# Kernel tuning notes

Measured on AMD Instinct MI355X. Metric: run time of the kernel, lower is better.

## Reference

```python
import jax, jax.numpy as jnp
import numpy as np

ALPHA = 1.0  # DPMConfig.alpha
N, D, K = 4096, 256, 64


def setup_inputs() -> dict:
    key = jax.random.key(0)
    k1, k2, k3, k4 = jax.random.split(key, 4)
    x = jax.random.normal(k1, (N, D), dtype=jnp.float32)
    means = jax.random.normal(k2, (K, D), dtype=jnp.float32)
    # SPD covariances: A A^T / D + 0.5 I
    A = jax.random.normal(k3, (K, D, D), dtype=jnp.float32)
    covs = jnp.einsum('kde,kfe->kdf', A, A) / D + 0.5 * jnp.eye(D, dtype=jnp.float32)
    counts = jax.random.uniform(k4, (K,), dtype=jnp.float32, minval=1.0, maxval=200.0)
    n_points = 100000
    return {"x": x, "means": means, "covs": covs, "counts": counts, "n_points": n_points}


def reference(x, means, covs, counts, n_points):
    n, d = x.shape
    k = means.shape[0]
    # deviations from every cluster mean: [N, K, D]
    dev = x[:, None, :] - means[None, :, :]
    # batched Mahalanobis solve: covs broadcast over points
    solved = jnp.linalg.solve(covs[None], dev[..., None])[..., 0]  # [N, K, D]
    quad = jnp.sum(dev * solved, axis=-1)  # [N, K]
    # logdet with the same jitter as the original
    _, log_dets = jnp.linalg.slogdet(covs + 1e-10 * jnp.eye(d, dtype=covs.dtype))  # [K]
    log_lik = -0.5 * (d * jnp.log(2.0 * jnp.pi) + log_dets[None, :] + quad)  # [N, K]
    denom = jnp.asarray(n_points, jnp.float32) + ALPHA
    log_prior = jnp.log(counts / denom)  # [K]
    log_new = jnp.log(ALPHA / denom)
    log_probs = jnp.concatenate(
        [log_lik + log_prior[None, :], jnp.full((n, 1), log_new, dtype=x.dtype)], axis=1
    )  # [N, K+1]
    # stable normalize (max-subtract + exp + sum == softmax)
    probs = jax.nn.softmax(log_probs, axis=1)
    return probs
```

## Files before the change

### kernel.cpp

```cpp
#include <hip/hip_runtime.h>
#include <math.h>


#define DD 256
#define KC 64
#define NPTS 4096
#define NT 64
#define BB 64
#define KG 4
#define CH 8
#define NCH (DD / CH)

__global__ __launch_bounds__(512) void pivot_kernel(
    const float* __restrict__ covs, float* __restrict__ S,
    float* __restrict__ Plbuf, float* __restrict__ ldp, int bs)
{
  const int k = blockIdx.x;
  const int by = blockIdx.y;
  const int tid = threadIdx.x;
  float* Pb = Plbuf + (size_t)k * BB * BB;

  __shared__ __align__(16) float Tl[BB][BB + 4];
  __shared__ __align__(16) float pivc[2][BB];
  __shared__ __align__(16) float pivr[2][BB];

  if (by < 4) {
    if (bs == 0) return;
    const int j0p = (bs - 1) * BB;
    const int r0 = by * BB;
    const float* src = ((bs == 1) ? covs : (const float*)S) + (size_t)k * DD * DD;
    float* dst = S + (size_t)k * DD * DD;

    const int rr = tid >> 3;
    const int cc = (tid & 7) * 8;
    *reinterpret_cast<float4*>(&Tl[rr][cc]) =
        *reinterpret_cast<const float4*>(&Pb[rr * BB + cc]);
    *reinterpret_cast<float4*>(&Tl[rr][cc + 4]) =
        *reinterpret_cast<const float4*>(&Pb[rr * BB + cc + 4]);
    __syncthreads();

    const int r = r0 + rr;
    if (r0 == j0p) {
      *reinterpret_cast<float4*>(&dst[(size_t)r * DD + j0p + cc]) =
          *reinterpret_cast<const float4*>(&Tl[rr][cc]);
      *reinterpret_cast<float4*>(&dst[(size_t)r * DD + j0p + cc + 4]) =
          *reinterpret_cast<const float4*>(&Tl[rr][cc + 4]);
    } else {
      float Crow[BB];
      #pragma unroll
      for (int p = 0; p < BB; p += 4) {
        float4 cv = *reinterpret_cast<const float4*>(&src[(size_t)r * DD + j0p + p]);
        Crow[p] = cv.x; Crow[p + 1] = cv.y; Crow[p + 2] = cv.z; Crow[p + 3] = cv.w;
      }
      float acc[8] = {0.f, 0.f, 0.f, 0.f, 0.f, 0.f, 0.f, 0.f};
      #pragma unroll
      for (int p = 0; p < BB; ++p) {
        float4 t0 = *reinterpret_cast<const float4*>(&Tl[p][cc]);
        float4 t1 = *reinterpret_cast<const float4*>(&Tl[p][cc + 4]);
        acc[0] = fmaf(Crow[p], t0.x, acc[0]);
        acc[1] = fmaf(Crow[p], t0.y, acc[1]);
        acc[2] = fmaf(Crow[p], t0.z, acc[2]);
        acc[3] = fmaf(Crow[p], t0.w, acc[3]);
        acc[4] = fmaf(Crow[p], t1.x, acc[4]);
        acc[5] = fmaf(Crow[p], t1.y, acc[5]);
        acc[6] = fmaf(Crow[p], t1.z, acc[6]);
        acc[7] = fmaf(Crow[p], t1.w, acc[7]);
      }
      float4 o0 = {-acc[0], -acc[1], -acc[2], -acc[3]};
      float4 o1 = {-acc[4], -acc[5], -acc[6], -acc[7]};
      *reinterpret_cast<float4*>(&dst[(size_t)r * DD + j0p + cc]) = o0;
      *reinterpret_cast<float4*>(&dst[(size_t)r * DD + j0p + cc + 4]) = o1;
    }
    return;
  }

  if (bs == 4) return;

  const int j0 = bs * BB;
  const float* psrc = ((bs == 0) ? covs : (const float*)S) + (size_t)k * DD * DD;
  const int pr = tid >> 3;
  const int pc = (tid & 7) * 8;

  float v[8];
  {
    float4 a4 = *reinterpret_cast<const float4*>(&psrc[(size_t)(j0 + pr) * DD + j0 + pc]);
    float4 b4 = *reinterpret_cast<const float4*>(&psrc[(size_t)(j0 + pr) * DD + j0 + pc + 4]);
    v[0] = a4.x; v[1] = a4.y; v[2] = a4.z; v[3] = a4.w;
    v[4] = b4.x; v[5] = b4.y; v[6] = b4.z; v[7] = b4.w;
  }
  if (pc == 0) pivc[0][pr] = v[0];
  if (pr == 0) {
    #pragma unroll
    for (int e = 0; e < 8; ++e) pivr[0][pc + e] = v[e];
  }
  __syncthreads();

  float ld = 0.0f;
  #pragma unroll 1
  for (int p = 0; p < BB; ++p) {
    const int cur = p & 1, nxt = cur ^ 1;
    const float d = pivc[cur][p];
    const float inv_d = 1.0f / d;
    if (tid == 0) ld += logf(d);
    const float cr = pivc[cur][pr];
    float rw[8];
    *reinterpret_cast<float4*>(&rw[0]) = *reinterpret_cast<const float4*>(&pivr[cur][pc]);
    *reinterpret_cast<float4*>(&rw[4]) = *reinterpret_cast<const float4*>(&pivr[cur][pc + 4]);
    #pragma unroll
    for (int e = 0; e < 8; ++e) {
      float ge = fmaf(-inv_d * cr, rw[e], v[e]);
      if (pr == p)     ge = rw[e] * inv_d;
      if (pc + e == p) ge = (pr == p) ? -inv_d : cr * inv_d;
      v[e] = ge;
    }
    if (p < BB - 1) {
      if (pr == p + 1) {
        #pragma unroll
        for (int e = 0; e < 8; ++e) pivr[nxt][pc + e] = v[e];
      }
      if (pc <= p + 1 && p + 1 < pc + 8) pivc[nxt][pr] = v[p + 1 - pc];
    }
    __syncthreads();
  }

  float4 s0 = {v[0], v[1], v[2], v[3]};
  float4 s1 = {v[4], v[5], v[6], v[7]};
  *reinterpret_cast<float4*>(&Pb[pr * BB + pc]) = s0;
  *reinterpret_cast<float4*>(&Pb[pr * BB + pc + 4]) = s1;
  if (tid == 0) ldp[bs * KC + k] = ld;
}

__global__ __launch_bounds__(512) void update_kernel(
    const float* __restrict__ covs, float* __restrict__ S,
    const float* __restrict__ Plbuf, int bs)
{
  const int k = blockIdx.x;
  const int si = blockIdx.y;
  const int t = si + (si >= bs ? 1 : 0);
  const int c0 = t * BB;
  const int j0 = bs * BB;
  const int tid = threadIdx.x;
  const float* src = ((bs == 0) ? covs : (const float*)S) + (size_t)k * DD * DD;
  float* dst = S + (size_t)k * DD * DD;

  __shared__ __align__(16) float Pl[BB][BB + 4];
  __shared__ __align__(16) float SJ[BB][BB + 4];
  __shared__ __align__(16) float Tl[BB][BB + 4];

  const float* Pb = Plbuf + (size_t)k * BB * BB;
  #pragma unroll
  for (int q = 0; q < 8; ++q) {
    int e = q * 512 + tid;
    int r = e >> 6, c = e & 63;
    Pl[r][c] = Pb[e];
    SJ[r][c] = src[(size_t)(j0 + r) * DD + c0 + c];
  }
  __syncthreads();

  {
    const int c = tid & 63;
    const int rg = (tid >> 6) * 8;
    float tv[8];
    #pragma unroll
    for (int r = 0; r < 8; ++r) tv[r] = 0.0f;
    for (int p = 0; p < BB; p += 4) {
      float s0 = SJ[p][c], s1 = SJ[p + 1][c], s2 = SJ[p + 2][c], s3 = SJ[p + 3][c];
      #pragma unroll
      for (int r = 0; r < 8; ++r) {
        float4 pv = *reinterpret_cast<const float4*>(&Pl[rg + r][p]);
        tv[r] = fmaf(pv.x, s0, fmaf(pv.y, s1, fmaf(pv.z, s2, fmaf(pv.w, s3, tv[r]))));
      }
    }
    #pragma unroll
    for (int r = 0; r < 8; ++r) Tl[rg + r][c] = tv[r];
  }
  __syncthreads();

  const int r = tid & 255;
  const int h = (tid >> 8) * 32;
  const bool inJ = (r >= j0) && (r < j0 + BB);
  if (inJ) {
    #pragma unroll
    for (int c = 0; c < 32; c += 4) {
      float4 tv4 = *reinterpret_cast<const float4*>(&Tl[r - j0][h + c]);
      float4 o = {-tv4.x, -tv4.y, -tv4.z, -tv4.w};
      *reinterpret_cast<float4*>(&dst[(size_t)r * DD + c0 + h + c]) = o;
    }
  } else {
    float Crow[BB];
    #pragma unroll
    for (int p = 0; p < BB; p += 4) {
      float4 cv = *reinterpret_cast<const float4*>(&src[(size_t)r * DD + j0 + p]);
      Crow[p] = cv.x; Crow[p + 1] = cv.y; Crow[p + 2] = cv.z; Crow[p + 3] = cv.w;
    }
    #pragma unroll
    for (int c = 0; c < 32; c += 4) {
      float4 acc = *reinterpret_cast<const float4*>(&src[(size_t)r * DD + c0 + h + c]);
      #pragma unroll
      for (int p = 0; p < BB; ++p) {
        float4 tv4 = *reinterpret_cast<const float4*>(&Tl[p][h + c]);
        acc.x = fmaf(Crow[p], tv4.x, acc.x);
        acc.y = fmaf(Crow[p], tv4.y, acc.y);
        acc.z = fmaf(Crow[p], tv4.z, acc.z);
        acc.w = fmaf(Crow[p], tv4.w, acc.w);
      }
      *reinterpret_cast<float4*>(&dst[(size_t)r * DD + c0 + h + c]) = acc;
    }
  }
}

__global__ __launch_bounds__(256) void w_kernel(
    const float* __restrict__ S, const float* __restrict__ means,
    const float* __restrict__ counts, const int* __restrict__ n_points_p,
    const float* __restrict__ ldp, float* __restrict__ cA,
    float* __restrict__ wv)
{
  const int k = blockIdx.x;
  const int tid = threadIdx.x;
  if (tid == 0) {
    float denom = (float)(*n_points_p) + 1.0f;
    float ld = ldp[k] + ldp[KC + k] + ldp[2 * KC + k] + ldp[3 * KC + k];
    cA[k] = logf(counts[k] / denom) - 0.5f * (470.49652900079047f + ld);
  }
  const float* Sk = S + (size_t)k * DD * DD;
  __shared__ float mus[DD];
  mus[tid] = means[(size_t)k * DD + tid];
  __syncthreads();
  float a0 = 0.f, a1 = 0.f, a2 = 0.f, a3 = 0.f;
  for (int j = 0; j < DD; j += 4) {
    a0 = fmaf(Sk[(size_t)(j + 0) * DD + tid], mus[j + 0], a0);
    a1 = fmaf(Sk[(size_t)(j + 1) * DD + tid], mus[j + 1], a1);
    a2 = fmaf(Sk[(size_t)(j + 2) * DD + tid], mus[j + 2], a2);
    a3 = fmaf(Sk[(size_t)(j + 3) * DD + tid], mus[j + 3], a3);
  }
  wv[(size_t)k * DD + tid] = (a0 + a1) + (a2 + a3);
}

__global__ __launch_bounds__(256) void quad_kernel(
    const float* __restrict__ X, const float* __restrict__ means,
    const float* __restrict__ S, const float* __restrict__ cA,
    const float* __restrict__ wv, float* __restrict__ lp)
{
  __shared__ __align__(16) float XT[DD][NT];
  __shared__ __align__(16) float Pl[CH * DD];
  __shared__ __align__(16) float muw[2][DD];
  __shared__ __align__(16) float lpb[KG][NT];

  const int tid = threadIdx.x;
  const int n0 = blockIdx.x * NT;
  const int k0 = blockIdx.y * KG;

  #pragma unroll
  for (int q = 0; q < 16; ++q) {
    int f = q * 1024 + tid * 4;
    int r = f >> 8;
    int c = f & 255;
    float4 xv = *reinterpret_cast<const float4*>(X + (size_t)(n0 + r) * DD + c);
    int rs = r ^ (((c >> 2) & 15) << 2);
    XT[c + 0][rs] = xv.x;
    XT[c + 1][rs] = xv.y;
    XT[c + 2][rs] = xv.z;
    XT[c + 3][rs] = xv.w;
  }

  const int tn = tid & 7;
  const int tj = tid >> 3;
  const int f0 = tid * 4;
  const int f1 = 1024 + tid * 4;

  #pragma unroll 1
  for (int kk = 0; kk < KG; ++kk) {
    const int k = k0 + kk;
    const float* Sk = S + (size_t)k * DD * DD;

    __syncthreads();
    muw[0][tid] = means[(size_t)k * DD + tid];
    muw[1][tid] = wv[(size_t)k * DD + tid];

    float4 pre0 = *reinterpret_cast<const float4*>(Sk + f0);
    float4 pre1 = *reinterpret_cast<const float4*>(Sk + f1);

    float y[8][8];
    #pragma unroll
    for (int a = 0; a < 8; ++a)
      #pragma unroll
      for (int b = 0; b < 8; ++b) y[a][b] = 0.0f;

    #pragma unroll 1
    for (int ct = 0; ct < NCH; ++ct) {
      __syncthreads();
      *reinterpret_cast<float4*>(&Pl[f0]) = pre0;
      *reinterpret_cast<float4*>(&Pl[f1]) = pre1;
      if (ct < NCH - 1) {
        const float* srcp = Sk + (size_t)(ct + 1) * CH * DD;
        pre0 = *reinterpret_cast<const float4*>(srcp + f0);
        pre1 = *reinterpret_cast<const float4*>(srcp + f1);
      }
      __syncthreads();

      #pragma unroll
      for (int il = 0; il < CH; ++il) {
        const int i = ct * CH + il;
        const int sw = ((i >> 2) & 15) << 2;
        float xv[8], pv[8];
        *reinterpret_cast<float4*>(&xv[0]) =
            *reinterpret_cast<const float4*>(&XT[i][(tn * 8) ^ sw]);
        *reinterpret_cast<float4*>(&xv[4]) =
            *reinterpret_cast<const float4*>(&XT[i][(tn * 8 + 4) ^ sw]);
        *reinterpret_cast<float4*>(&pv[0]) =
            *reinterpret_cast<const float4*>(&Pl[il * DD + tj * 8]);
        *reinterpret_cast<float4*>(&pv[4]) =
            *reinterpret_cast<const float4*>(&Pl[il * DD + tj * 8 + 4]);
        #pragma unroll
        for (int a = 0; a < 8; ++a)
          #pragma unroll
          for (int b = 0; b < 8; ++b)
            y[a][b] = fmaf(xv[a], pv[b], y[a][b]);
      }
    }

    float s[8];
    #pragma unroll
    for (int a = 0; a < 8; ++a) s[a] = 0.0f;
    #pragma unroll
    for (int b = 0; b < 8; ++b) {
      const int j = tj * 8 + b;
      const int swj = ((j >> 2) & 15) << 2;
      float dv[8];
      *reinterpret_cast<float4*>(&dv[0]) =
          *reinterpret_cast<const float4*>(&XT[j][(tn * 8) ^ swj]);
      *reinterpret_cast<float4*>(&dv[4]) =
          *reinterpret_cast<const float4*>(&XT[j][(tn * 8 + 4) ^ swj]);
      const float mj = muw[0][j];
      const float wj = muw[1][j];
      #pragma unroll
      for (int a = 0; a < 8; ++a)
        s[a] = fmaf(dv[a] - mj, y[a][b] - wj, s[a]);
    }

    float* qred = &Pl[0];
    __syncthreads();
    *reinterpret_cast<float4*>(&qred[tj * 64 + tn * 8]) =
        *reinterpret_cast<const float4*>(&s[0]);
    *reinterpret_cast<float4*>(&qred[tj * 64 + tn * 8 + 4]) =
        *reinterpret_cast<const float4*>(&s[4]);
    __syncthreads();
    if (tid < 64) {
      float qa = 0.f, qb = 0.f, qc = 0.f, qd = 0.f;
      #pragma unroll
      for (int t = 0; t < 32; t += 4) {
        qa += qred[(t + 0) * 64 + tid];
        qb += qred[(t + 1) * 64 + tid];
        qc += qred[(t + 2) * 64 + tid];
        qd += qred[(t + 3) * 64 + tid];
      }
      lpb[kk][tid] = fmaf(0.5f, (qa + qb) + (qc + qd), cA[k]);
    }
  }

  __syncthreads();
  if (tid < 64) {
    float4 o = {lpb[0][tid], lpb[1][tid], lpb[2][tid], lpb[3][tid]};
    *reinterpret_cast<float4*>(&lp[(size_t)(n0 + tid) * KC + k0]) = o;
  }
}

__global__ __launch_bounds__(64) void softmax_kernel(
    const float* __restrict__ lp, const int* __restrict__ n_points_p,
    float* __restrict__ out)
{
  const int n = blockIdx.x;
  const int l = threadIdx.x;
  const float denom = (float)(*n_points_p) + 1.0f;
  const float log_new = -logf(denom);

  float v = lp[(size_t)n * KC + l];
  float m = v;
  #pragma unroll
  for (int off = 32; off > 0; off >>= 1) m = fmaxf(m, __shfl_xor(m, off, 64));
  m = fmaxf(m, log_new);

  float e = expf(v - m);
  float s = e;
  #pragma unroll
  for (int off = 32; off > 0; off >>= 1) s += __shfl_xor(s, off, 64);
  float enew = expf(log_new - m);
  s += enew;

  out[(size_t)n * (KC + 1) + l] = e / s;
  if (l == 0) out[(size_t)n * (KC + 1) + KC] = enew / s;
}

extern "C" void kernel_launch(void* const* d_in, const int* in_sizes, int n_in,
                              void* d_out, int out_size, void* d_ws, size_t ws_size,
                              hipStream_t stream)
{
  const float* x       = (const float*)d_in[0];
  const float* means   = (const float*)d_in[1];
  const float* covs    = (const float*)d_in[2];
  const float* counts  = (const float*)d_in[3];
  const int*   n_points = (const int*)d_in[4];

  float* S   = (float*)d_ws;
  float* cA  = S + (size_t)KC * DD * DD;
  float* ldp = cA + KC;
  float* lp  = ldp + 4 * KC;
  float* Plbuf = lp;
  float* out = (float*)d_out;
  float* wv = out;

  for (int bs = 0; bs < 4; ++bs) {
    pivot_kernel<<<dim3(KC, 5), 512, 0, stream>>>(covs, S, Plbuf, ldp, bs);
    update_kernel<<<dim3(KC, 3), 512, 0, stream>>>(covs, S, Plbuf, bs);
  }
  pivot_kernel<<<dim3(KC, 5), 512, 0, stream>>>(covs, S, Plbuf, ldp, 4);
  w_kernel<<<KC, 256, 0, stream>>>(S, means, counts, n_points, ldp, cA, wv);
  quad_kernel<<<dim3(NPTS / NT, KC / KG), 256, 0, stream>>>(x, means, S, cA, wv, lp);
  softmax_kernel<<<NPTS, 64, 0, stream>>>(lp, n_points, out);
}
```

Measured before the change: 648.2 us.

## Fuse blocked covariance inversion sweep and w computation into one cooperative kernel

Replaces the nine pivot/update kernel launches and the separate w_kernel with a single cooperative kernel of 4 blocks per cluster, using grid-wide syncs between phases. Each block redundantly computes the 64x64 pivot inverse in shared memory, so the pivot block no longer round-trips through a global buffer and the per-step log-determinants accumulate in registers. The w = S*mu product is also split across the 4 blocks per cluster instead of one. This removes launch gaps and global staging at the cost of duplicated pivot work, grid-sync latency, and a co-residency requirement of 256 blocks of 512 threads.

```diff
diff --git a/kernel.cpp b/kernel.cpp
--- a/kernel.cpp
+++ b/kernel.cpp
@@ -1,5 +1,8 @@
 #include <hip/hip_runtime.h>
+#include <hip/hip_cooperative_groups.h>
 #include <math.h>
+
+namespace cg = cooperative_groups;
 
 
 #define DD 256
@@ -11,229 +14,217 @@
 #define CH 8
 #define NCH (DD / CH)
 
-__global__ __launch_bounds__(512) void pivot_kernel(
-    const float* __restrict__ covs, float* __restrict__ S,
-    float* __restrict__ Plbuf, float* __restrict__ ldp, int bs)
+__global__ __launch_bounds__(512) void sweep_coop(
+    const float* __restrict__ covs, const float* __restrict__ counts,
+    const int* __restrict__ n_points_p, float* __restrict__ S,
+    float* __restrict__ cA, const float* __restrict__ means,
+    float* __restrict__ wv)
 {
-  const int k = blockIdx.x;
-  const int by = blockIdx.y;
+  cg::grid_group gg = cg::this_grid();
+  const int bid = blockIdx.x;
+  const int k = bid & (KC - 1);
+  const int ro = bid >> 6;
   const int tid = threadIdx.x;
-  float* Pb = Plbuf + (size_t)k * BB * BB;
-
+  float* Sk = S + (size_t)k * DD * DD;
+  const float* Ck = covs + (size_t)k * DD * DD;
+
+  __shared__ __align__(16) float Pl[BB][BB + 4];
+  __shared__ __align__(16) float SJ[BB][BB + 4];
   __shared__ __align__(16) float Tl[BB][BB + 4];
   __shared__ __align__(16) float pivc[2][BB];
   __shared__ __align__(16) float pivr[2][BB];
 
-  if (by < 4) {
-    if (bs == 0) return;
-    const int j0p = (bs - 1) * BB;
-    const int r0 = by * BB;
-    const float* src = ((bs == 1) ? covs : (const float*)S) + (size_t)k * DD * DD;
-    float* dst = S + (size_t)k * DD * DD;
-
-    const int rr = tid >> 3;
-    const int cc = (tid & 7) * 8;
-    *reinterpret_cast<float4*>(&Tl[rr][cc]) =
-        *reinterpret_cast<const float4*>(&Pb[rr * BB + cc]);
-    *reinterpret_cast<float4*>(&Tl[rr][cc + 4]) =
-        *reinterpret_cast<const float4*>(&Pb[rr * BB + cc + 4]);
-    __syncthreads();
-
-    const int r = r0 + rr;
-    if (r0 == j0p) {
-      *reinterpret_cast<float4*>(&dst[(size_t)r * DD + j0p + cc]) =
-          *reinterpret_cast<const float4*>(&Tl[rr][cc]);
-      *reinterpret_cast<float4*>(&dst[(size_t)r * DD + j0p + cc + 4]) =
-          *reinterpret_cast<const float4*>(&Tl[rr][cc + 4]);
-    } else {
-      float Crow[BB];
-      #pragma unroll
-      for (int p = 0; p < BB; p += 4) {
-        float4 cv = *reinterpret_cast<const float4*>(&src[(size_t)r * DD + j0p + p]);
-        Crow[p] = cv.x; Crow[p + 1] = cv.y; Crow[p + 2] = cv.z; Crow[p + 3] = cv.w;
-      }
-      float acc[8] = {0.f, 0.f, 0.f, 0.f, 0.f, 0.f, 0.f, 0.f};
-      #pragma unroll
-      for (int p = 0; p < BB; ++p) {
-        float4 t0 = *reinterpret_cast<const float4*>(&Tl[p][cc]);
-        float4 t1 = *reinterpret_cast<const float4*>(&Tl[p][cc + 4]);
-        acc[0] = fmaf(Crow[p], t0.x, acc[0]);
-        acc[1] = fmaf(Crow[p], t0.y, acc[1]);
-        acc[2] = fmaf(Crow[p], t0.z, acc[2]);
-        acc[3] = fmaf(Crow[p], t0.w, acc[3]);
-        acc[4] = fmaf(Crow[p], t1.x, acc[4]);
-        acc[5] = fmaf(Crow[p], t1.y, acc[5]);
-        acc[6] = fmaf(Crow[p], t1.z, acc[6]);
-        acc[7] = fmaf(Crow[p], t1.w, acc[7]);
-      }
-      float4 o0 = {-acc[0], -acc[1], -acc[2], -acc[3]};
-      float4 o1 = {-acc[4], -acc[5], -acc[6], -acc[7]};
-      *reinterpret_cast<float4*>(&dst[(size_t)r * DD + j0p + cc]) = o0;
-      *reinterpret_cast<float4*>(&dst[(size_t)r * DD + j0p + cc + 4]) = o1;
-    }
-    return;
-  }
-
-  if (bs == 4) return;
-
-  const int j0 = bs * BB;
-  const float* psrc = ((bs == 0) ? covs : (const float*)S) + (size_t)k * DD * DD;
+  float ld_acc = 0.0f;
+
   const int pr = tid >> 3;
   const int pc = (tid & 7) * 8;
 
-  float v[8];
+  for (int bs = 0; bs < 5; ++bs) {
+    if (bs > 0) {
+      const int j0p = (bs - 1) * BB;
+      const float* dsrc = (bs == 1) ? Ck : (const float*)Sk;
+      const int rr = tid >> 3;
+      const int cc = (tid & 7) * 8;
+      const int r = ro * BB + rr;
+      if (ro == bs - 1) {
+        *reinterpret_cast<float4*>(&Sk[(size_t)r * DD + j0p + cc]) =
+            *reinterpret_cast<const float4*>(&Pl[rr][cc]);
+        *reinterpret_cast<float4*>(&Sk[(size_t)r * DD + j0p + cc + 4]) =
+            *reinterpret_cast<const float4*>(&Pl[rr][cc + 4]);
+      } else {
+        float Crow[BB];
+        #pragma unroll
+        for (int p = 0; p < BB; p += 4) {
+          float4 cv = *reinterpret_cast<const float4*>(&dsrc[(size_t)r * DD + j0p + p]);
+          Crow[p] = cv.x; Crow[p + 1] = cv.y; Crow[p + 2] = cv.z; Crow[p + 3] = cv.w;
+        }
+        float acc[8] = {0.f, 0.f, 0.f, 0.f, 0.f, 0.f, 0.f, 0.f};
+        #pragma unroll
+        for (int p = 0; p < BB; ++p) {
+          float4 t0 = *reinterpret_cast<const float4*>(&Pl[p][cc]);
+          float4 t1 = *reinterpret_cast<const float4*>(&Pl[p][cc + 4]);
+          acc[0] = fmaf(Crow[p], t0.x, acc[0]);
+          acc[1] = fmaf(Crow[p], t0.y, acc[1]);
+          acc[2] = fmaf(Crow[p], t0.z, acc[2]);
+          acc[3] = fmaf(Crow[p], t0.w, acc[3]);
+          acc[4] = fmaf(Crow[p], t1.x, acc[4]);
+          acc[5] = fmaf(Crow[p], t1.y, acc[5]);
+          acc[6] = fmaf(Crow[p], t1.z, acc[6]);
+          acc[7] = fmaf(Crow[p], t1.w, acc[7]);
+        }
+        float4 o0 = {-acc[0], -acc[1], -acc[2], -acc[3]};
+        float4 o1 = {-acc[4], -acc[5], -acc[6], -acc[7]};
+        *reinterpret_cast<float4*>(&Sk[(size_t)r * DD + j0p + cc]) = o0;
+        *reinterpret_cast<float4*>(&Sk[(size_t)r * DD + j0p + cc + 4]) = o1;
+      }
+    }
+    if (bs == 4) break;
+
+    {
+      const int j0 = bs * BB;
+      const float* psrc = (bs == 0) ? Ck : (const float*)Sk;
+      float v[8];
+      {
+        float4 a4 = *reinterpret_cast<const float4*>(&psrc[(size_t)(j0 + pr) * DD + j0 + pc]);
+        float4 b4 = *reinterpret_cast<const float4*>(&psrc[(size_t)(j0 + pr) * DD + j0 + pc + 4]);
+        v[0] = a4.x; v[1] = a4.y; v[2] = a4.z; v[3] = a4.w;
+        v[4] = b4.x; v[5] = b4.y; v[6] = b4.z; v[7] = b4.w;
+      }
+      if (pc == 0) pivc[0][pr] = v[0];
+      if (pr == 0) {
+        #pragma unroll
+        for (int e = 0; e < 8; ++e) pivr[0][pc + e] = v[e];
+      }
+      __syncthreads();
+
+      float ld = 0.0f;
+      #pragma unroll 1
+      for (int p = 0; p < BB; ++p) {
+        const int cur = p & 1, nxt = cur ^ 1;
+        const float d = pivc[cur][p];
+        const float inv_d = 1.0f / d;
+        if (tid == 0) ld += logf(d);
+        const float cr = pivc[cur][pr];
+        float rw[8];
+        *reinterpret_cast<float4*>(&rw[0]) = *reinterpret_cast<const float4*>(&pivr[cur][pc]);
+        *reinterpret_cast<float4*>(&rw[4]) = *reinterpret_cast<const float4*>(&pivr[cur][pc + 4]);
+        #pragma unroll
+        for (int e = 0; e < 8; ++e) {
+          float ge = fmaf(-inv_d * cr, rw[e], v[e]);
+          if (pr == p)     ge = rw[e] * inv_d;
+          if (pc + e == p) ge = (pr == p) ? -inv_d : cr * inv_d;
+          v[e] = ge;
+        }
+        if (p < BB - 1) {
+          if (pr == p + 1) {
+            #pragma unroll
+            for (int e = 0; e < 8; ++e) pivr[nxt][pc + e] = v[e];
+          }
+          if (pc <= p + 1 && p + 1 < pc + 8) pivc[nxt][pr] = v[p + 1 - pc];
+        }
+        __syncthreads();
+      }
+      *reinterpret_cast<float4*>(&Pl[pr][pc]) = *reinterpret_cast<const float4*>(&v[0]);
+      *reinterpret_cast<float4*>(&Pl[pr][pc + 4]) = *reinterpret_cast<const float4*>(&v[4]);
+      if (tid == 0) ld_acc += ld;
+      __syncthreads();
+    }
+    gg.sync();
+
+    if (ro != bs) {
+      const int c0 = ro * BB;
+      const int j0 = bs * BB;
+      const float* src = (bs == 0) ? Ck : (const float*)Sk;
+
+      #pragma unroll
+      for (int q = 0; q < 8; ++q) {
+        int e = q * 512 + tid;
+        int r = e >> 6, c = e & 63;
+        SJ[r][c] = src[(size_t)(j0 + r) * DD + c0 + c];
+      }
+      __syncthreads();
+
+      {
+        const int c = tid & 63;
+        const int rg = (tid >> 6) * 8;
+        float tv[8];
+        #pragma unroll
+        for (int r = 0; r < 8; ++r) tv[r] = 0.0f;
+        for (int p = 0; p < BB; p += 4) {
+          float s0 = SJ[p][c], s1 = SJ[p + 1][c], s2 = SJ[p + 2][c], s3 = SJ[p + 3][c];
+          #pragma unroll
+          for (int r = 0; r < 8; ++r) {
+            float4 pv = *reinterpret_cast<const float4*>(&Pl[rg + r][p]);
+            tv[r] = fmaf(pv.x, s0, fmaf(pv.y, s1, fmaf(pv.z, s2, fmaf(pv.w, s3, tv[r]))));
+          }
+        }
+        #pragma unroll
+        for (int r = 0; r < 8; ++r) Tl[rg + r][c] = tv[r];
+      }
+      __syncthreads();
+
+      const int r = tid & 255;
+      const int h = (tid >> 8) * 32;
+      const bool inJ = (r >= j0) && (r < j0 + BB);
+      if (inJ) {
+        #pragma unroll
+        for (int c = 0; c < 32; c += 4) {
+          float4 tv4 = *reinterpret_cast<const float4*>(&Tl[r - j0][h + c]);
+          float4 o = {-tv4.x, -tv4.y, -tv4.z, -tv4.w};
+          *reinterpret_cast<float4*>(&Sk[(size_t)r * DD + c0 + h + c]) = o;
+        }
+      } else {
+        float Crow[BB];
+        #pragma unroll
+        for (int p = 0; p < BB; p += 4) {
+          float4 cv = *reinterpret_cast<const float4*>(&src[(size_t)r * DD + j0 + p]);
+          Crow[p] = cv.x; Crow[p + 1] = cv.y; Crow[p + 2] = cv.z; Crow[p + 3] = cv.w;
+        }
+        #pragma unroll
+        for (int c = 0; c < 32; c += 4) {
+          float4 acc = *reinterpret_cast<const float4*>(&src[(size_t)r * DD + c0 + h + c]);
+          #pragma unroll
+          for (int p = 0; p < BB; ++p) {
+            float4 tv4 = *reinterpret_cast<const float4*>(&Tl[p][h + c]);
+            acc.x = fmaf(Crow[p], tv4.x, acc.x);
+            acc.y = fmaf(Crow[p], tv4.y, acc.y);
+            acc.z = fmaf(Crow[p], tv4.z, acc.z);
+            acc.w = fmaf(Crow[p], tv4.w, acc.w);
+          }
+          *reinterpret_cast<float4*>(&Sk[(size_t)r * DD + c0 + h + c]) = acc;
+        }
+      }
+      __syncthreads();
+    }
+    gg.sync();
+  }
+  gg.sync();
+
   {
-    float4 a4 = *reinterpret_cast<const float4*>(&psrc[(size_t)(j0 + pr) * DD + j0 + pc]);
-    float4 b4 = *reinterpret_cast<const float4*>(&psrc[(size_t)(j0 + pr) * DD + j0 + pc + 4]);
-    v[0] = a4.x; v[1] = a4.y; v[2] = a4.z; v[3] = a4.w;
-    v[4] = b4.x; v[5] = b4.y; v[6] = b4.z; v[7] = b4.w;
+    float* muL = &SJ[0][0];
+    if (tid < DD) muL[tid] = means[(size_t)k * DD + tid];
+    __syncthreads();
+    const int jj = tid & 63;
+    const int p = tid >> 6;
+    float acc = 0.0f;
+    const float* Sc = Sk + (size_t)(p * 32) * DD + ro * BB + jj;
+    #pragma unroll 4
+    for (int i = 0; i < 32; ++i)
+      acc = fmaf(Sc[(size_t)i * DD], muL[p * 32 + i], acc);
+    float* red = &Tl[0][0];
+    red[p * 64 + jj] = acc;
+    __syncthreads();
+    if (tid < 64) {
+      float t = 0.0f;
+      #pragma unroll
+      for (int q = 0; q < 8; ++q) t += red[q * 64 + tid];
+      wv[(size_t)k * DD + ro * BB + tid] = t;
+    }
+    if (ro == 0 && tid == 0) {
+      float denom = (float)(*n_points_p) + 1.0f;
+      cA[k] = logf(counts[k] / denom) - 0.5f * (470.49652900079047f + ld_acc);
+    }
   }
-  if (pc == 0) pivc[0][pr] = v[0];
-  if (pr == 0) {
-    #pragma unroll
-    for (int e = 0; e < 8; ++e) pivr[0][pc + e] = v[e];
-  }
-  __syncthreads();
-
-  float ld = 0.0f;
-  #pragma unroll 1
-  for (int p = 0; p < BB; ++p) {
-    const int cur = p & 1, nxt = cur ^ 1;
-    const float d = pivc[cur][p];
-    const float inv_d = 1.0f / d;
-    if (tid == 0) ld += logf(d);
-    const float cr = pivc[cur][pr];
-    float rw[8];
-    *reinterpret_cast<float4*>(&rw[0]) = *reinterpret_cast<const float4*>(&pivr[cur][pc]);
-    *reinterpret_cast<float4*>(&rw[4]) = *reinterpret_cast<const float4*>(&pivr[cur][pc + 4]);
-    #pragma unroll
-    for (int e = 0; e < 8; ++e) {
-      float ge = fmaf(-inv_d * cr, rw[e], v[e]);
-      if (pr == p)     ge = rw[e] * inv_d;
-      if (pc + e == p) ge = (pr == p) ? -inv_d : cr * inv_d;
-      v[e] = ge;
-    }
-    if (p < BB - 1) {
-      if (pr == p + 1) {
-        #pragma unroll
-        for (int e = 0; e < 8; ++e) pivr[nxt][pc + e] = v[e];
-      }
-      if (pc <= p + 1 && p + 1 < pc + 8) pivc[nxt][pr] = v[p + 1 - pc];
-    }
-    __syncthreads();
-  }
-
-  float4 s0 = {v[0], v[1], v[2], v[3]};
-  float4 s1 = {v[4], v[5], v[6], v[7]};
-  *reinterpret_cast<float4*>(&Pb[pr * BB + pc]) = s0;
-  *reinterpret_cast<float4*>(&Pb[pr * BB + pc + 4]) = s1;
-  if (tid == 0) ldp[bs * KC + k] = ld;
-}
-
-__global__ __launch_bounds__(512) void update_kernel(
-    const float* __restrict__ covs, float* __restrict__ S,
-    const float* __restrict__ Plbuf, int bs)
-{
-  const int k = blockIdx.x;
-  const int si = blockIdx.y;
-  const int t = si + (si >= bs ? 1 : 0);
-  const int c0 = t * BB;
-  const int j0 = bs * BB;
-  const int tid = threadIdx.x;
-  const float* src = ((bs == 0) ? covs : (const float*)S) + (size_t)k * DD * DD;
-  float* dst = S + (size_t)k * DD * DD;
-
-  __shared__ __align__(16) float Pl[BB][BB + 4];
-  __shared__ __align__(16) float SJ[BB][BB + 4];
-  __shared__ __align__(16) float Tl[BB][BB + 4];
-
-  const float* Pb = Plbuf + (size_t)k * BB * BB;
-  #pragma unroll
-  for (int q = 0; q < 8; ++q) {
-    int e = q * 512 + tid;
-    int r = e >> 6, c = e & 63;
-    Pl[r][c] = Pb[e];
-    SJ[r][c] = src[(size_t)(j0 + r) * DD + c0 + c];
-  }
-  __syncthreads();
-
-  {
-    const int c = tid & 63;
-    const int rg = (tid >> 6) * 8;
-    float tv[8];
-    #pragma unroll
-    for (int r = 0; r < 8; ++r) tv[r] = 0.0f;
-    for (int p = 0; p < BB; p += 4) {
-      float s0 = SJ[p][c], s1 = SJ[p + 1][c], s2 = SJ[p + 2][c], s3 = SJ[p + 3][c];
-      #pragma unroll
-      for (int r = 0; r < 8; ++r) {
-        float4 pv = *reinterpret_cast<const float4*>(&Pl[rg + r][p]);
-        tv[r] = fmaf(pv.x, s0, fmaf(pv.y, s1, fmaf(pv.z, s2, fmaf(pv.w, s3, tv[r]))));
-      }
-    }
-    #pragma unroll
-    for (int r = 0; r < 8; ++r) Tl[rg + r][c] = tv[r];
-  }
-  __syncthreads();
-
-  const int r = tid & 255;
-  const int h = (tid >> 8) * 32;
-  const bool inJ = (r >= j0) && (r < j0 + BB);
-  if (inJ) {
-    #pragma unroll
-    for (int c = 0; c < 32; c += 4) {
-      float4 tv4 = *reinterpret_cast<const float4*>(&Tl[r - j0][h + c]);
-      float4 o = {-tv4.x, -tv4.y, -tv4.z, -tv4.w};
-      *reinterpret_cast<float4*>(&dst[(size_t)r * DD + c0 + h + c]) = o;
-    }
-  } else {
-    float Crow[BB];
-    #pragma unroll
-    for (int p = 0; p < BB; p += 4) {
-      float4 cv = *reinterpret_cast<const float4*>(&src[(size_t)r * DD + j0 + p]);
-      Crow[p] = cv.x; Crow[p + 1] = cv.y; Crow[p + 2] = cv.z; Crow[p + 3] = cv.w;
-    }
-    #pragma unroll
-    for (int c = 0; c < 32; c += 4) {
-      float4 acc = *reinterpret_cast<const float4*>(&src[(size_t)r * DD + c0 + h + c]);
-      #pragma unroll
-      for (int p = 0; p < BB; ++p) {
-        float4 tv4 = *reinterpret_cast<const float4*>(&Tl[p][h + c]);
-        acc.x = fmaf(Crow[p], tv4.x, acc.x);
-        acc.y = fmaf(Crow[p], tv4.y, acc.y);
-        acc.z = fmaf(Crow[p], tv4.z, acc.z);
-        acc.w = fmaf(Crow[p], tv4.w, acc.w);
-      }
-      *reinterpret_cast<float4*>(&dst[(size_t)r * DD + c0 + h + c]) = acc;
-    }
-  }
-}
-
-__global__ __launch_bounds__(256) void w_kernel(
-    const float* __restrict__ S, const float* __restrict__ means,
-    const float* __restrict__ counts, const int* __restrict__ n_points_p,
-    const float* __restrict__ ldp, float* __restrict__ cA,
-    float* __restrict__ wv)
-{
-  const int k = blockIdx.x;
-  const int tid = threadIdx.x;
-  if (tid == 0) {
-    float denom = (float)(*n_points_p) + 1.0f;
-    float ld = ldp[k] + ldp[KC + k] + ldp[2 * KC + k] + ldp[3 * KC + k];
-    cA[k] = logf(counts[k] / denom) - 0.5f * (470.49652900079047f + ld);
-  }
-  const float* Sk = S + (size_t)k * DD * DD;
-  __shared__ float mus[DD];
-  mus[tid] = means[(size_t)k * DD + tid];
-  __syncthreads();
-  float a0 = 0.f, a1 = 0.f, a2 = 0.f, a3 = 0.f;
-  for (int j = 0; j < DD; j += 4) {
-    a0 = fmaf(Sk[(size_t)(j + 0) * DD + tid], mus[j + 0], a0);
-    a1 = fmaf(Sk[(size_t)(j + 1) * DD + tid], mus[j + 1], a1);
-    a2 = fmaf(Sk[(size_t)(j + 2) * DD + tid], mus[j + 2], a2);
-    a3 = fmaf(Sk[(size_t)(j + 3) * DD + tid], mus[j + 3], a3);
-  }
-  wv[(size_t)k * DD + tid] = (a0 + a1) + (a2 + a3);
 }
 
 __global__ __launch_bounds__(256) void quad_kernel(
@@ -401,20 +392,16 @@
   const float* counts  = (const float*)d_in[3];
   const int*   n_points = (const int*)d_in[4];
 
-  float* S   = (float*)d_ws;
-  float* cA  = S + (size_t)KC * DD * DD;
-  float* ldp = cA + KC;
-  float* lp  = ldp + 4 * KC;
-  float* Plbuf = lp;
+  float* S  = (float*)d_ws;
+  float* cA = S + (size_t)KC * DD * DD;
+  float* lp = cA + KC;
   float* out = (float*)d_out;
   float* wv = out;
 
-  for (int bs = 0; bs < 4; ++bs) {
-    pivot_kernel<<<dim3(KC, 5), 512, 0, stream>>>(covs, S, Plbuf, ldp, bs);
-    update_kernel<<<dim3(KC, 3), 512, 0, stream>>>(covs, S, Plbuf, bs);
-  }
-  pivot_kernel<<<dim3(KC, 5), 512, 0, stream>>>(covs, S, Plbuf, ldp, 4);
-  w_kernel<<<KC, 256, 0, stream>>>(S, means, counts, n_points, ldp, cA, wv);
+  void* args[] = {(void*)&covs, (void*)&counts, (void*)&n_points,
+                  (void*)&S, (void*)&cA, (void*)&means, (void*)&wv};
+  hipLaunchCooperativeKernel(sweep_coop, dim3(4 * KC), dim3(512), args, 0, stream);
+
   quad_kernel<<<dim3(NPTS / NT, KC / KG), 256, 0, stream>>>(x, means, S, cA, wv, lp);
   softmax_kernel<<<NPTS, 64, 0, stream>>>(lp, n_points, out);
 }
```

New measurement: 1.091 ms. 1.68x slower.

## Give each wavefront a private double-buffered S tile to drop block barriers

Applied to the files above, without the earlier changes.

The shared staging of S rows in quad_kernel is restructured. Each 64-lane wavefront now stages only the 64 columns it consumes, four rows at a time, into its own padded double buffer. This removes the two block-wide __syncthreads per 8-row chunk in the inner reduction loop and depends on in-wave lockstep ordering of LDS writes and reads. The trade-offs are more, smaller chunks with a prefetch distance of one chunk, and a correctness assumption that wave64 execution keeps the buffer handoff safe without barriers.

```diff
diff --git a/kernel.cpp b/kernel.cpp
--- a/kernel.cpp
+++ b/kernel.cpp
@@ -8,8 +8,6 @@
 #define NT 64
 #define BB 64
 #define KG 4
-#define CH 8
-#define NCH (DD / CH)
 
 __global__ __launch_bounds__(512) void pivot_kernel(
     const float* __restrict__ covs, float* __restrict__ S,
@@ -242,7 +240,7 @@
     const float* __restrict__ wv, float* __restrict__ lp)
 {
   __shared__ __align__(16) float XT[DD][NT];
-  __shared__ __align__(16) float Pl[CH * DD];
+  __shared__ __align__(16) float Pw[4][2][4][68];
   __shared__ __align__(16) float muw[2][DD];
   __shared__ __align__(16) float lpb[KG][NT];
 
@@ -265,20 +263,24 @@
 
   const int tn = tid & 7;
   const int tj = tid >> 3;
-  const int f0 = tid * 4;
-  const int f1 = 1024 + tid * 4;
+  const int wid = tid >> 6;
+  const int lane = tid & 63;
+  const int g = (tid >> 3) & 7;
+  const int srow = lane >> 4;
+  const int scol = (lane & 15) * 4;
 
   #pragma unroll 1
   for (int kk = 0; kk < KG; ++kk) {
     const int k = k0 + kk;
-    const float* Sk = S + (size_t)k * DD * DD;
+    const float* Skw = S + (size_t)k * DD * DD + wid * 64;
 
     __syncthreads();
     muw[0][tid] = means[(size_t)k * DD + tid];
     muw[1][tid] = wv[(size_t)k * DD + tid];
 
-    float4 pre0 = *reinterpret_cast<const float4*>(Sk + f0);
-    float4 pre1 = *reinterpret_cast<const float4*>(Sk + f1);
+    float4 st = *reinterpret_cast<const float4*>(Skw + (size_t)srow * DD + scol);
+    *reinterpret_cast<float4*>(&Pw[wid][0][srow][scol]) = st;
+    st = *reinterpret_cast<const float4*>(Skw + (size_t)(4 + srow) * DD + scol);
 
     float y[8][8];
     #pragma unroll
@@ -287,20 +289,11 @@
       for (int b = 0; b < 8; ++b) y[a][b] = 0.0f;
 
     #pragma unroll 1
-    for (int ct = 0; ct < NCH; ++ct) {
-      __syncthreads();
-      *reinterpret_cast<float4*>(&Pl[f0]) = pre0;
-      *reinterpret_cast<float4*>(&Pl[f1]) = pre1;
-      if (ct < NCH - 1) {
-        const float* srcp = Sk + (size_t)(ct + 1) * CH * DD;
-        pre0 = *reinterpret_cast<const float4*>(srcp + f0);
-        pre1 = *reinterpret_cast<const float4*>(srcp + f1);
-      }
-      __syncthreads();
-
-      #pragma unroll
-      for (int il = 0; il < CH; ++il) {
-        const int i = ct * CH + il;
+    for (int ct = 0; ct < 64; ++ct) {
+      const int cur = ct & 1;
+      #pragma unroll
+      for (int il = 0; il < 4; ++il) {
+        const int i = ct * 4 + il;
         const int sw = ((i >> 2) & 15) << 2;
         float xv[8], pv[8];
         *reinterpret_cast<float4*>(&xv[0]) =
@@ -308,16 +301,23 @@
         *reinterpret_cast<float4*>(&xv[4]) =
             *reinterpret_cast<const float4*>(&XT[i][(tn * 8 + 4) ^ sw]);
         *reinterpret_cast<float4*>(&pv[0]) =
-            *reinterpret_cast<const float4*>(&Pl[il * DD + tj * 8]);
+            *reinterpret_cast<const float4*>(&Pw[wid][cur][il][g * 8]);
         *reinterpret_cast<float4*>(&pv[4]) =
-            *reinterpret_cast<const float4*>(&Pl[il * DD + tj * 8 + 4]);
+            *reinterpret_cast<const float4*>(&Pw[wid][cur][il][g * 8 + 4]);
         #pragma unroll
         for (int a = 0; a < 8; ++a)
           #pragma unroll
           for (int b = 0; b < 8; ++b)
             y[a][b] = fmaf(xv[a], pv[b], y[a][b]);
       }
-    }
+      if (ct < 63) {
+        *reinterpret_cast<float4*>(&Pw[wid][cur ^ 1][srow][scol]) = st;
+        const int cnx = (ct + 2 < 64) ? (ct + 2) : 63;
+        st = *reinterpret_cast<const float4*>(
+            Skw + (size_t)(cnx * 4 + srow) * DD + scol);
+      }
+    }
+    __syncthreads();
 
     float s[8];
     #pragma unroll
@@ -338,8 +338,7 @@
         s[a] = fmaf(dv[a] - mj, y[a][b] - wj, s[a]);
     }
 
-    float* qred = &Pl[0];
-    __syncthreads();
+    float* qred = &Pw[0][0][0][0];
     *reinterpret_cast<float4*>(&qred[tj * 64 + tn * 8]) =
         *reinterpret_cast<const float4*>(&s[0]);
     *reinterpret_cast<float4*>(&qred[tj * 64 + tn * 8 + 4]) =
```

Measured after the change: 628.1 us. 3.1% less time.
